# Kernel tuning notes

Hardware: AMD Instinct MI355X
Metric: run time of the kernel (lower is better)

## Reference

```python
import jax, jax.numpy as jnp
import numpy as np

RPN_SCALES = (2.0, 4.0, 8.0, 16.0)   # feature-map strides per pyramid level
BASE_SIZES = (8.0, 16.0, 32.0, 64.0) # rpn_base_sizes: nearest-size level assignment
CROP_SIZE = 14                        # output crop resolution
IMG = 512


def setup_inputs() -> dict:
    key = jax.random.key(0)
    kf0, kf1, kf2, kf3, kx, ky, ks, ka, ksc = jax.random.split(key, 9)
    C = 256
    f0 = jax.random.normal(kf0, (1, C, 256, 256), dtype=jnp.float32)
    f1 = jax.random.normal(kf1, (1, C, 128, 128), dtype=jnp.float32)
    f2 = jax.random.normal(kf2, (1, C, 64, 64), dtype=jnp.float32)
    f3 = jax.random.normal(kf3, (1, C, 32, 32), dtype=jnp.float32)

    N = 1024
    # box sizes log-uniform in [4, 128] so every pyramid level is exercised
    s = 2.0 ** jax.random.uniform(ks, (N,), minval=2.0, maxval=7.0)
    ar = jax.random.uniform(ka, (N,), minval=0.7, maxval=1.4)
    w = s * jnp.sqrt(ar)
    h = s / jnp.sqrt(ar)
    x0 = jax.random.uniform(kx, (N,), minval=0.0, maxval=IMG - 1.0 - 128.0)
    y0 = jax.random.uniform(ky, (N,), minval=0.0, maxval=IMG - 1.0 - 128.0)
    x1 = jnp.minimum(x0 + w, IMG - 1.0)
    y1 = jnp.minimum(y0 + h, IMG - 1.0)
    score = jax.random.uniform(ksc, (N,))
    bidx = jnp.zeros((N,), dtype=jnp.float32)  # single image in batch
    proposals = jnp.stack([bidx, x0, y0, x1, y1, score, jnp.zeros((N,))], axis=1).astype(jnp.float32)
    return {"f0": f0, "f1": f1, "f2": f2, "f3": f3, "proposals": proposals}


def _roi_crop(f, rois, stride):
    """ROIAlign-style bilinear crop. f: [B,C,H,W], rois: [N,5] (b,x0,y0,x1,y1 image coords).
    Returns [N, C, S, S]."""
    S = CROP_SIZE
    H, W = f.shape[2], f.shape[3]
    b = rois[:, 0].astype(jnp.int32)
    x0, y0, x1, y1 = (rois[:, i] / stride for i in (1, 2, 3, 4))
    bw = (x1 - x0) / S
    bh = (y1 - y0) / S
    grid = jnp.arange(S, dtype=f.dtype) + 0.5
    xs = x0[:, None] + grid[None, :] * bw[:, None] - 0.5   # [N,S] sample centers
    ys = y0[:, None] + grid[None, :] * bh[:, None] - 0.5

    def split(coord, M):
        c0 = jnp.floor(coord)
        frac = coord - c0
        i0 = jnp.clip(c0.astype(jnp.int32), 0, M - 1)
        i1 = jnp.clip(i0 + 1, 0, M - 1)
        return i0, i1, frac

    yi0, yi1, wy = split(ys, H)
    xi0, xi1, wx = split(xs, W)
    bb = b[:, None, None]                                   # [N,1,1]

    def g(yi, xi):
        # advanced indexing with middle slice -> [N,S,S,C]
        return f[bb, :, yi[:, :, None], xi[:, None, :]]

    wy = wy[:, :, None, None]                               # [N,S,1,1]
    wx = wx[:, None, :, None]                               # [N,1,S,1]
    v = (g(yi0, xi0) * (1 - wy) * (1 - wx)
         + g(yi0, xi1) * (1 - wy) * wx
         + g(yi1, xi0) * wy * (1 - wx)
         + g(yi1, xi1) * wy * wx)                            # [N,S,S,C]
    return jnp.transpose(v, (0, 3, 1, 2))                   # [N,C,S,S]


def reference(f0, f1, f2, f3, proposals):
    boxes = proposals[:, 1:5]
    sizes = jnp.sqrt((boxes[:, 2] - boxes[:, 0]) * (boxes[:, 3] - boxes[:, 1]))
    dist = jnp.abs(sizes[:, None] - jnp.asarray(BASE_SIZES, dtype=sizes.dtype)[None, :])
    min_index = jnp.argmin(dist, axis=1)                    # per-proposal level assignment
    rois = proposals[:, 0:5]
    # route -> compute -> combine, expressed as compute-all-levels + per-proposal select
    # (identical math to gather-per-level + sort-restore in the original)
    crops_all = jnp.stack([_roi_crop(f, rois, s)
                           for f, s in zip((f0, f1, f2, f3), RPN_SCALES)])  # [L,N,C,S,S]
    return crops_all[min_index, jnp.arange(rois.shape[0])]  # [N,C,S,S]
```

## Files before the change

kernel.cpp:

```cpp
#include <hip/hip_runtime.h>

#define CROP_S 14
#define NPIX   196
#define NCH    256
#define CPB    16
#define NGRP   (NCH / CPB)
#define PROWS  12
#define PCOLS  16
#define PSZ    (PROWS * PCOLS)
#define STAGE_V4 (CPB * PSZ / 4)
#define OUTV4  (CPB * NPIX / 4)
#define QPC    (NPIX / 4)

typedef float v4f __attribute__((ext_vector_type(4)));

__global__ __launch_bounds__(256) void roi_crop_kernel(
    const float* __restrict__ f0, const float* __restrict__ f1,
    const float* __restrict__ f2, const float* __restrict__ f3,
    const float* __restrict__ proposals, float* __restrict__ out)
{
    __shared__ float s_patch[CPB * PSZ];
    __shared__ int   s_o00[NPIX];
    __shared__ float s_wx[NPIX], s_wy[NPIX];

    const int bid = blockIdx.x;
    const int n   = bid >> 4;
    const int cg  = bid & (NGRP - 1);
    const int c0  = cg * CPB;
    const int tid = threadIdx.x;

    const float px0 = proposals[n * 7 + 1];
    const float py0 = proposals[n * 7 + 2];
    const float px1 = proposals[n * 7 + 3];
    const float py1 = proposals[n * 7 + 4];

    const float size = sqrtf((px1 - px0) * (py1 - py0));
    int lvl = 0;
    float bd = fabsf(size - 8.0f);
    {
        float d1 = fabsf(size - 16.0f);
        if (d1 < bd) { bd = d1; lvl = 1; }
        float d2 = fabsf(size - 32.0f);
        if (d2 < bd) { bd = d2; lvl = 2; }
        float d3 = fabsf(size - 64.0f);
        if (d3 < bd) { bd = d3; lvl = 3; }
    }

    const float* f = (lvl == 0) ? f0 : (lvl == 1) ? f1 : (lvl == 2) ? f2 : f3;
    const float stride = (float)(2 << lvl);
    const int   M      = 256 >> lvl;
    const int   HW     = M * M;

    const float x0s = px0 / stride, y0s = py0 / stride;
    const float x1s = px1 / stride, y1s = py1 / stride;
    const float bw = (x1s - x0s) / (float)CROP_S;
    const float bh = (y1s - y0s) / (float)CROP_S;

    const int ylo  = min(max((int)floorf(y0s + 0.5f * bh - 0.5f), 0), M - 1);
    int xlo4 = min(max((int)floorf(x0s + 0.5f * bw - 0.5f), 0), M - 1) & ~3;
    xlo4 = min(xlo4, M - PCOLS);

    {
        const float* fbase = f + (size_t)c0 * HW + xlo4;
        #pragma unroll
        for (int it = 0; it < STAGE_V4 / 256; ++it) {
            const int sidx = it * 256 + tid;
            const int c    = sidx / (PSZ / 4);
            const int rem  = sidx - c * (PSZ / 4);
            const int r    = rem >> 2;
            const int q    = rem & 3;
            const int gy   = min(ylo + r, M - 1);
            const v4f v = *reinterpret_cast<const v4f*>(
                fbase + (size_t)c * HW + gy * M + q * 4);
            *reinterpret_cast<v4f*>(&s_patch[sidx * 4]) = v;
        }
    }

    if (tid < NPIX) {
        const int y = tid / CROP_S;
        const int x = tid - y * CROP_S;
        const float xs = x0s + ((float)x + 0.5f) * bw - 0.5f;
        const float ys = y0s + ((float)y + 0.5f) * bh - 0.5f;
        const float fx = floorf(xs), fy = floorf(ys);
        s_wx[tid] = xs - fx;
        s_wy[tid] = ys - fy;
        const int xi0 = min(max((int)fx, 0), M - 1);
        const int yi0 = min(max((int)fy, 0), M - 1);
        const int ci0 = min(xi0 - xlo4, PCOLS - 2);
        const int ri0 = min(yi0 - ylo,  PROWS - 2);
        s_o00[tid] = ri0 * PCOLS + ci0;
    }
    __syncthreads();

    v4f* ob = reinterpret_cast<v4f*>(
        out + (size_t)n * (NCH * NPIX) + (size_t)c0 * NPIX);
    #pragma unroll
    for (int i = 0; i < 4; ++i) {
        const int idx4 = i * 256 + tid;
        if (idx4 < OUTV4) {
            const int c  = idx4 / QPC;
            const int pq = idx4 - c * QPC;
            const int p0 = pq * 4;
            const float* pp = s_patch + c * PSZ;
            v4f v;
            #pragma unroll
            for (int j = 0; j < 4; ++j) {
                const int   p  = p0 + j;
                const int   o  = s_o00[p];
                const float wx = s_wx[p];
                const float wy = s_wy[p];
                const float v00 = pp[o],         v01 = pp[o + 1];
                const float v10 = pp[o + PCOLS], v11 = pp[o + PCOLS + 1];
                const float r0 = v00 + wx * (v01 - v00);
                const float r1 = v10 + wx * (v11 - v10);
                v[j] = r0 + wy * (r1 - r0);
            }
            ob[idx4] = v;
        }
    }
}

extern "C" void kernel_launch(void* const* d_in, const int* in_sizes, int n_in,
                              void* d_out, int out_size, void* d_ws, size_t ws_size,
                              hipStream_t stream) {
    const float* f0 = (const float*)d_in[0];
    const float* f1 = (const float*)d_in[1];
    const float* f2 = (const float*)d_in[2];
    const float* f3 = (const float*)d_in[3];
    const float* proposals = (const float*)d_in[4];
    float* out = (float*)d_out;

    const int N = in_sizes[4] / 7;

    roi_crop_kernel<<<dim3(N * NGRP), dim3(256), 0, stream>>>(f0, f1, f2, f3, proposals, out);
}
```

Measured before the change: 67.90 us.

## Make each wavefront own its channel slice and drop block-wide barrier

Each block now handles 32 channels, split so that each of its four wavefronts stages and interpolates its own 8 channels in a private LDS region. This removes the __syncthreads and the shared per-pixel offset and weight tables. Those values are recomputed per lane inside the interpolation loop, and outputs are written with nontemporal stores. The grid shrinks by half, and each lane now does extra ALU work for the index math.

```diff
diff --git a/kernel.cpp b/kernel.cpp
--- a/kernel.cpp
+++ b/kernel.cpp
@@ -3,13 +3,15 @@
 #define CROP_S 14
 #define NPIX   196
 #define NCH    256
-#define CPB    16
+#define CPW    8
+#define WVS    4
+#define CPB    (CPW * WVS)
 #define NGRP   (NCH / CPB)
 #define PROWS  12
 #define PCOLS  16
 #define PSZ    (PROWS * PCOLS)
-#define STAGE_V4 (CPB * PSZ / 4)
-#define OUTV4  (CPB * NPIX / 4)
+#define WSTG   (CPW * PSZ / 4)
+#define WOUT   (CPW * NPIX / 4)
 #define QPC    (NPIX / 4)
 
 typedef float v4f __attribute__((ext_vector_type(4)));
@@ -19,15 +21,16 @@
     const float* __restrict__ f2, const float* __restrict__ f3,
     const float* __restrict__ proposals, float* __restrict__ out)
 {
-    __shared__ float s_patch[CPB * PSZ];
-    __shared__ int   s_o00[NPIX];
-    __shared__ float s_wx[NPIX], s_wy[NPIX];
+    __shared__ float s_patch[WVS * CPW * PSZ];
+
+    const int tid = threadIdx.x;
+    const int wv  = tid >> 6;
+    const int ln  = tid & 63;
 
     const int bid = blockIdx.x;
-    const int n   = bid >> 4;
+    const int n   = bid >> 3;
     const int cg  = bid & (NGRP - 1);
-    const int c0  = cg * CPB;
-    const int tid = threadIdx.x;
+    const int c0  = cg * CPB + wv * CPW;
 
     const float px0 = proposals[n * 7 + 1];
     const float py0 = proposals[n * 7 + 2];
@@ -60,62 +63,55 @@
     int xlo4 = min(max((int)floorf(x0s + 0.5f * bw - 0.5f), 0), M - 1) & ~3;
     xlo4 = min(xlo4, M - PCOLS);
 
+    float* wlds = s_patch + wv * (CPW * PSZ);
     {
         const float* fbase = f + (size_t)c0 * HW + xlo4;
         #pragma unroll
-        for (int it = 0; it < STAGE_V4 / 256; ++it) {
-            const int sidx = it * 256 + tid;
-            const int c    = sidx / (PSZ / 4);
-            const int rem  = sidx - c * (PSZ / 4);
+        for (int it = 0; it < WSTG / 64; ++it) {
+            const int sidx = it * 64 + ln;
+            const int c    = sidx / 48;
+            const int rem  = sidx - c * 48;
             const int r    = rem >> 2;
             const int q    = rem & 3;
             const int gy   = min(ylo + r, M - 1);
             const v4f v = *reinterpret_cast<const v4f*>(
                 fbase + (size_t)c * HW + gy * M + q * 4);
-            *reinterpret_cast<v4f*>(&s_patch[sidx * 4]) = v;
+            *reinterpret_cast<v4f*>(wlds + sidx * 4) = v;
         }
     }
-
-    if (tid < NPIX) {
-        const int y = tid / CROP_S;
-        const int x = tid - y * CROP_S;
-        const float xs = x0s + ((float)x + 0.5f) * bw - 0.5f;
-        const float ys = y0s + ((float)y + 0.5f) * bh - 0.5f;
-        const float fx = floorf(xs), fy = floorf(ys);
-        s_wx[tid] = xs - fx;
-        s_wy[tid] = ys - fy;
-        const int xi0 = min(max((int)fx, 0), M - 1);
-        const int yi0 = min(max((int)fy, 0), M - 1);
-        const int ci0 = min(xi0 - xlo4, PCOLS - 2);
-        const int ri0 = min(yi0 - ylo,  PROWS - 2);
-        s_o00[tid] = ri0 * PCOLS + ci0;
-    }
-    __syncthreads();
 
     v4f* ob = reinterpret_cast<v4f*>(
         out + (size_t)n * (NCH * NPIX) + (size_t)c0 * NPIX);
     #pragma unroll
-    for (int i = 0; i < 4; ++i) {
-        const int idx4 = i * 256 + tid;
-        if (idx4 < OUTV4) {
+    for (int it = 0; it < 7; ++it) {
+        const int idx4 = it * 64 + ln;
+        if (idx4 < WOUT) {
             const int c  = idx4 / QPC;
-            const int pq = idx4 - c * QPC;
-            const int p0 = pq * 4;
-            const float* pp = s_patch + c * PSZ;
+            const int p0 = (idx4 - c * QPC) * 4;
+            const float* pp = wlds + c * PSZ;
             v4f v;
             #pragma unroll
             for (int j = 0; j < 4; ++j) {
-                const int   p  = p0 + j;
-                const int   o  = s_o00[p];
-                const float wx = s_wx[p];
-                const float wy = s_wy[p];
+                const int p  = p0 + j;
+                const int py = p / CROP_S;
+                const int px = p - py * CROP_S;
+                const float xs = x0s + ((float)px + 0.5f) * bw - 0.5f;
+                const float ys = y0s + ((float)py + 0.5f) * bh - 0.5f;
+                const float fx = floorf(xs), fy = floorf(ys);
+                const float wx = xs - fx;
+                const float wy = ys - fy;
+                const int xi0 = min(max((int)fx, 0), M - 1);
+                const int yi0 = min(max((int)fy, 0), M - 1);
+                const int ci0 = min(xi0 - xlo4, PCOLS - 2);
+                const int ri0 = min(yi0 - ylo,  PROWS - 2);
+                const int o   = ri0 * PCOLS + ci0;
                 const float v00 = pp[o],         v01 = pp[o + 1];
                 const float v10 = pp[o + PCOLS], v11 = pp[o + PCOLS + 1];
                 const float r0 = v00 + wx * (v01 - v00);
                 const float r1 = v10 + wx * (v11 - v10);
                 v[j] = r0 + wy * (r1 - r0);
             }
-            ob[idx4] = v;
+            __builtin_nontemporal_store(v, ob + idx4);
         }
     }
 }
```

After: 74.61 us. 1.1x slower.
